# Optimization experiments

Hardware: AMD Instinct MI355X
Metric: run time of the kernel (lower is better)

Reference implementation:

```python
import jax, jax.numpy as jnp
import numpy as np


def setup_inputs() -> dict:
    key = jax.random.key(0)
    x = jax.random.normal(key, (8192, 1024), dtype=jnp.float32)
    return {"x": x}


def reference(x):
    # attn_scores = x @ x.T  -> [N, N]
    scores = jnp.einsum('nd,md->nm', x, x)
    # softmax over last dim (stable)
    weights = jax.nn.softmax(scores, axis=-1)
    # context = weights @ x -> [N, d]
    return jnp.einsum('nm,md->nd', weights, x)
```

## Files before the change

### kernel.cpp

```cpp
#include <hip/hip_runtime.h>
#include <hip/hip_bf16.h>
#include <cstdint>

#define NROWS 8192
#define DDIM  1024
#define QBLK  32
#define KVT   128
#define DC    64
#define NW    8
#define NITER (NROWS / KVT)
#define NDC   (DDIM / DC)
#define LOG2E 1.44269504088896340736f

typedef __attribute__((ext_vector_type(4))) float f32x4;
typedef __attribute__((ext_vector_type(8))) short bf16x8;
typedef unsigned short u16;

__device__ __forceinline__ u16 f2bf(float f) {
  uint32_t u = __builtin_bit_cast(uint32_t, f);
  uint32_t r = u + 0x7FFFu + ((u >> 16) & 1u);
  return (u16)(r >> 16);
}

__global__ __launch_bounds__(256) void prep_kernel(const float* __restrict__ x,
                                                   u16* __restrict__ xbf,
                                                   u16* __restrict__ xbfT) {
  __shared__ __align__(16) u16 T[64][72];
  const int t = threadIdx.x;
  const int n0 = blockIdx.x * 64;
  const int d0 = blockIdx.y * 64;
#pragma unroll
  for (int rr = 0; rr < 4; ++rr) {
    const int row = (t >> 4) + rr * 16;
    const int c4 = (t & 15) * 4;
    const float4 v = *reinterpret_cast<const float4*>(&x[(size_t)(n0 + row) * DDIM + d0 + c4]);
    ushort4 b;
    b.x = f2bf(v.x); b.y = f2bf(v.y); b.z = f2bf(v.z); b.w = f2bf(v.w);
    *reinterpret_cast<ushort4*>(&xbf[(size_t)(n0 + row) * DDIM + d0 + c4]) = b;
    *reinterpret_cast<ushort4*>(&T[row][c4]) = b;
  }
  __syncthreads();
#pragma unroll
  for (int rr = 0; rr < 4; ++rr) {
    const int drow = (t >> 4) + rr * 16;
    const int nc = (t & 15) * 4;
    ushort4 o;
    o.x = T[nc + 0][drow]; o.y = T[nc + 1][drow];
    o.z = T[nc + 2][drow]; o.w = T[nc + 3][drow];
    *reinterpret_cast<ushort4*>(&xbfT[(size_t)(d0 + drow) * NROWS + n0 + nc]) = o;
  }
}

__global__ __launch_bounds__(512, 2) void attn_kernel(const u16* __restrict__ xbf,
                                                      const u16* __restrict__ xbfT,
                                                      float* __restrict__ out) {
  __shared__ __align__(16) u16 Qs[2][QBLK][DC + 8];
  __shared__ __align__(16) u16 Ks[2][KVT][DC + 8];
  __shared__ __align__(16) u16 Ps[QBLK][KVT + 8];
  __shared__ float smax[NW][QBLK];
  __shared__ float ssum[NW][QBLK];

  const int tid = threadIdx.x;
  const int w = tid >> 6;
  const int lane = tid & 63;
  const int g = lane >> 4;
  const int ln16 = lane & 15;
  const int j = lane & 31;
  const int q0 = blockIdx.x * QBLK;

  const int kr = tid >> 2, kc = (tid & 3) * 16;
  const int qr = tid >> 4, qc = (tid & 15) * 4;

  int4 rk0, rk1; ushort4 rq;

  auto load_chunk = [&](int t_, int dc_) {
    const size_t ko = (size_t)(t_ * KVT + kr) * DDIM + dc_ * DC + kc;
    rk0 = *reinterpret_cast<const int4*>(&xbf[ko]);
    rk1 = *reinterpret_cast<const int4*>(&xbf[ko + 8]);
    const size_t qo = (size_t)(q0 + qr) * DDIM + dc_ * DC + qc;
    rq = *reinterpret_cast<const ushort4*>(&xbf[qo]);
  };
  auto write_chunk = [&](int buf) {
    *reinterpret_cast<int4*>(&Ks[buf][kr][kc]) = rk0;
    *reinterpret_cast<int4*>(&Ks[buf][kr][kc + 8]) = rk1;
    *reinterpret_cast<ushort4*>(&Qs[buf][qr][qc]) = rq;
  };

  f32x4 oacc[2][8];
#pragma unroll
  for (int f = 0; f < 2; ++f)
#pragma unroll
    for (int c = 0; c < 8; ++c) oacc[f][c] = (f32x4){0.f, 0.f, 0.f, 0.f};
  float m_run = -INFINITY, l_run = 0.0f;

  load_chunk(0, 0);

  for (int t = 0; t < NITER; ++t) {
    f32x4 sacc[2] = {{0.f,0.f,0.f,0.f},{0.f,0.f,0.f,0.f}};
    for (int dc = 0; dc < NDC; ++dc) {
      const int buf = dc & 1;
      write_chunk(buf);
      if (dc + 1 < NDC) load_chunk(t, dc + 1);
      else if (t + 1 < NITER) load_chunk(t + 1, 0);
      __syncthreads();
#pragma unroll
      for (int kk = 0; kk < 2; ++kk) {
        const int kq = kk * 32 + g * 8;
        bf16x8 a0 = *reinterpret_cast<const bf16x8*>(&Qs[buf][ln16][kq]);
        bf16x8 a1 = *reinterpret_cast<const bf16x8*>(&Qs[buf][16 + ln16][kq]);
        bf16x8 b  = *reinterpret_cast<const bf16x8*>(&Ks[buf][w * 16 + ln16][kq]);
        sacc[0] = __builtin_amdgcn_mfma_f32_16x16x32_bf16(a0, b, sacc[0], 0, 0, 0);
        sacc[1] = __builtin_amdgcn_mfma_f32_16x16x32_bf16(a1, b, sacc[1], 0, 0, 0);
      }
    }

    float rmx[2][4];
#pragma unroll
    for (int f = 0; f < 2; ++f)
#pragma unroll
      for (int r = 0; r < 4; ++r) {
        float v = sacc[f][r];
        v = fmaxf(v, __shfl_xor(v, 1, 16));
        v = fmaxf(v, __shfl_xor(v, 2, 16));
        v = fmaxf(v, __shfl_xor(v, 4, 16));
        v = fmaxf(v, __shfl_xor(v, 8, 16));
        rmx[f][r] = v;
      }
    if (ln16 == 0) {
#pragma unroll
      for (int f = 0; f < 2; ++f)
#pragma unroll
        for (int r = 0; r < 4; ++r) smax[w][f * 16 + g * 4 + r] = rmx[f][r];
    }
    __syncthreads();
    float tm = smax[0][j];
#pragma unroll
    for (int wv = 1; wv < NW; ++wv) tm = fmaxf(tm, smax[wv][j]);
    const float mnew = fmaxf(m_run, tm);
    const float alpha = exp2f((m_run - mnew) * LOG2E);
    m_run = mnew;

    float mrow[2][4], arow[2][4];
#pragma unroll
    for (int f = 0; f < 2; ++f)
#pragma unroll
      for (int r = 0; r < 4; ++r) {
        const int row = f * 16 + g * 4 + r;
        mrow[f][r] = __shfl(mnew, row);
        arow[f][r] = __shfl(alpha, row);
      }

    float prb[2][4], rs[2][4];
#pragma unroll
    for (int f = 0; f < 2; ++f)
#pragma unroll
      for (int r = 0; r < 4; ++r) {
        const float p = exp2f((sacc[f][r] - mrow[f][r]) * LOG2E);
        prb[f][r] = p;
        float s = p;
        s += __shfl_xor(s, 1, 16);
        s += __shfl_xor(s, 2, 16);
        s += __shfl_xor(s, 4, 16);
        s += __shfl_xor(s, 8, 16);
        rs[f][r] = s;
      }
    if (ln16 == 0) {
#pragma unroll
      for (int f = 0; f < 2; ++f)
#pragma unroll
        for (int r = 0; r < 4; ++r) ssum[w][f * 16 + g * 4 + r] = rs[f][r];
    }
#pragma unroll
    for (int f = 0; f < 2; ++f)
#pragma unroll
      for (int r = 0; r < 4; ++r)
        Ps[f * 16 + g * 4 + r][w * 16 + ln16] = f2bf(prb[f][r]);
    __syncthreads();

    float ts = ssum[0][j];
#pragma unroll
    for (int wv = 1; wv < NW; ++wv) ts += ssum[wv][j];
    l_run = l_run * alpha + ts;

#pragma unroll
    for (int f = 0; f < 2; ++f)
#pragma unroll
      for (int cf = 0; cf < 8; ++cf)
#pragma unroll
        for (int r = 0; r < 4; ++r) oacc[f][cf][r] *= arow[f][r];

    const int kvb = t * KVT;
#pragma unroll
    for (int kk = 0; kk < 4; ++kk) {
      bf16x8 pa0 = *reinterpret_cast<const bf16x8*>(&Ps[ln16][kk * 32 + g * 8]);
      bf16x8 pa1 = *reinterpret_cast<const bf16x8*>(&Ps[16 + ln16][kk * 32 + g * 8]);
#pragma unroll
      for (int cf = 0; cf < 8; ++cf) {
        const int c = w * 128 + cf * 16 + ln16;
        const int4 vv = *reinterpret_cast<const int4*>(
            &xbfT[(size_t)c * NROWS + kvb + kk * 32 + g * 8]);
        const bf16x8 vb = __builtin_bit_cast(bf16x8, vv);
        oacc[0][cf] = __builtin_amdgcn_mfma_f32_16x16x32_bf16(pa0, vb, oacc[0][cf], 0, 0, 0);
        oacc[1][cf] = __builtin_amdgcn_mfma_f32_16x16x32_bf16(pa1, vb, oacc[1][cf], 0, 0, 0);
      }
    }
  }

  const float rinv = 1.0f / l_run;
  float rrow[2][4];
#pragma unroll
  for (int f = 0; f < 2; ++f)
#pragma unroll
    for (int r = 0; r < 4; ++r) rrow[f][r] = __shfl(rinv, f * 16 + g * 4 + r);
#pragma unroll
  for (int f = 0; f < 2; ++f)
#pragma unroll
    for (int cf = 0; cf < 8; ++cf)
#pragma unroll
      for (int r = 0; r < 4; ++r) {
        const int row = q0 + f * 16 + g * 4 + r;
        const int c = w * 128 + cf * 16 + ln16;
        out[(size_t)row * DDIM + c] = oacc[f][cf][r] * rrow[f][r];
      }
}

extern "C" void kernel_launch(void* const* d_in, const int* in_sizes, int n_in,
                              void* d_out, int out_size, void* d_ws, size_t ws_size,
                              hipStream_t stream) {
  const float* x = (const float*)d_in[0];
  u16* xbf  = (u16*)d_ws;
  u16* xbfT = xbf + (size_t)NROWS * DDIM;
  float* out = (float*)d_out;

  hipLaunchKernelGGL(prep_kernel, dim3(NROWS / 64, DDIM / 64), dim3(256), 0, stream,
                     x, xbf, xbfT);
  hipLaunchKernelGGL(attn_kernel, dim3(NROWS / QBLK), dim3(512), 0, stream,
                     xbf, xbfT, out);
}
```

Baseline: 997.0 us.

## Halve query block, keep full Q tile resident in LDS, batch V loads

Reduces the query block from 32 to 16 rows, which doubles the grid to 512 blocks and raises the occupancy target to 4 blocks per CU. The whole 16x1024 Q tile is now loaded into LDS once, so the per-chunk Q streaming is gone. In the PV loop, all eight V fragments are loaded before the MFMAs run, and the MFMA section is wrapped in raised wave priority. The trade-off is that each K/V tile now serves half as many query rows, so global and L2 traffic for K and V roughly doubles.

```diff
diff --git a/kernel.cpp b/kernel.cpp
--- a/kernel.cpp
+++ b/kernel.cpp
@@ -4,7 +4,7 @@
 
 #define NROWS 8192
 #define DDIM  1024
-#define QBLK  32
+#define QBLK  16
 #define KVT   128
 #define DC    64
 #define NW    8
@@ -51,10 +51,10 @@
   }
 }
 
-__global__ __launch_bounds__(512, 2) void attn_kernel(const u16* __restrict__ xbf,
+__global__ __launch_bounds__(512, 4) void attn_kernel(const u16* __restrict__ xbf,
                                                       const u16* __restrict__ xbfT,
                                                       float* __restrict__ out) {
-  __shared__ __align__(16) u16 Qs[2][QBLK][DC + 8];
+  __shared__ __align__(16) u16 Qf[QBLK][DDIM + 8];
   __shared__ __align__(16) u16 Ks[2][KVT][DC + 8];
   __shared__ __align__(16) u16 Ps[QBLK][KVT + 8];
   __shared__ float smax[NW][QBLK];
@@ -65,38 +65,39 @@
   const int lane = tid & 63;
   const int g = lane >> 4;
   const int ln16 = lane & 15;
-  const int j = lane & 31;
   const int q0 = blockIdx.x * QBLK;
 
+  {
+    const int qr = tid >> 5;
+    const int qc0 = (tid & 31) * 32;
+#pragma unroll
+    for (int i = 0; i < 4; ++i) {
+      const int4 v = *reinterpret_cast<const int4*>(&xbf[(size_t)(q0 + qr) * DDIM + qc0 + i * 8]);
+      *reinterpret_cast<int4*>(&Qf[qr][qc0 + i * 8]) = v;
+    }
+  }
+
   const int kr = tid >> 2, kc = (tid & 3) * 16;
-  const int qr = tid >> 4, qc = (tid & 15) * 4;
-
-  int4 rk0, rk1; ushort4 rq;
-
+  int4 rk0, rk1;
   auto load_chunk = [&](int t_, int dc_) {
     const size_t ko = (size_t)(t_ * KVT + kr) * DDIM + dc_ * DC + kc;
     rk0 = *reinterpret_cast<const int4*>(&xbf[ko]);
     rk1 = *reinterpret_cast<const int4*>(&xbf[ko + 8]);
-    const size_t qo = (size_t)(q0 + qr) * DDIM + dc_ * DC + qc;
-    rq = *reinterpret_cast<const ushort4*>(&xbf[qo]);
   };
   auto write_chunk = [&](int buf) {
     *reinterpret_cast<int4*>(&Ks[buf][kr][kc]) = rk0;
     *reinterpret_cast<int4*>(&Ks[buf][kr][kc + 8]) = rk1;
-    *reinterpret_cast<ushort4*>(&Qs[buf][qr][qc]) = rq;
   };
 
-  f32x4 oacc[2][8];
-#pragma unroll
-  for (int f = 0; f < 2; ++f)
-#pragma unroll
-    for (int c = 0; c < 8; ++c) oacc[f][c] = (f32x4){0.f, 0.f, 0.f, 0.f};
+  f32x4 oacc[8];
+#pragma unroll
+  for (int c = 0; c < 8; ++c) oacc[c] = (f32x4){0.f, 0.f, 0.f, 0.f};
   float m_run = -INFINITY, l_run = 0.0f;
 
   load_chunk(0, 0);
 
   for (int t = 0; t < NITER; ++t) {
-    f32x4 sacc[2] = {{0.f,0.f,0.f,0.f},{0.f,0.f,0.f,0.f}};
+    f32x4 sacc = {0.f, 0.f, 0.f, 0.f};
     for (int dc = 0; dc < NDC; ++dc) {
       const int buf = dc & 1;
       write_chunk(buf);
@@ -105,123 +106,105 @@
       __syncthreads();
 #pragma unroll
       for (int kk = 0; kk < 2; ++kk) {
-        const int kq = kk * 32 + g * 8;
-        bf16x8 a0 = *reinterpret_cast<const bf16x8*>(&Qs[buf][ln16][kq]);
-        bf16x8 a1 = *reinterpret_cast<const bf16x8*>(&Qs[buf][16 + ln16][kq]);
-        bf16x8 b  = *reinterpret_cast<const bf16x8*>(&Ks[buf][w * 16 + ln16][kq]);
-        sacc[0] = __builtin_amdgcn_mfma_f32_16x16x32_bf16(a0, b, sacc[0], 0, 0, 0);
-        sacc[1] = __builtin_amdgcn_mfma_f32_16x16x32_bf16(a1, b, sacc[1], 0, 0, 0);
+        bf16x8 a = *reinterpret_cast<const bf16x8*>(&Qf[ln16][dc * DC + kk * 32 + g * 8]);
+        bf16x8 b = *reinterpret_cast<const bf16x8*>(&Ks[buf][w * 16 + ln16][kk * 32 + g * 8]);
+        sacc = __builtin_amdgcn_mfma_f32_16x16x32_bf16(a, b, sacc, 0, 0, 0);
       }
     }
 
-    float rmx[2][4];
-#pragma unroll
-    for (int f = 0; f < 2; ++f)
-#pragma unroll
-      for (int r = 0; r < 4; ++r) {
-        float v = sacc[f][r];
-        v = fmaxf(v, __shfl_xor(v, 1, 16));
-        v = fmaxf(v, __shfl_xor(v, 2, 16));
-        v = fmaxf(v, __shfl_xor(v, 4, 16));
-        v = fmaxf(v, __shfl_xor(v, 8, 16));
-        rmx[f][r] = v;
-      }
+    float rmx[4];
+#pragma unroll
+    for (int r = 0; r < 4; ++r) {
+      float v = sacc[r];
+      v = fmaxf(v, __shfl_xor(v, 1, 16));
+      v = fmaxf(v, __shfl_xor(v, 2, 16));
+      v = fmaxf(v, __shfl_xor(v, 4, 16));
+      v = fmaxf(v, __shfl_xor(v, 8, 16));
+      rmx[r] = v;
+    }
     if (ln16 == 0) {
 #pragma unroll
-      for (int f = 0; f < 2; ++f)
-#pragma unroll
-        for (int r = 0; r < 4; ++r) smax[w][f * 16 + g * 4 + r] = rmx[f][r];
+      for (int r = 0; r < 4; ++r) smax[w][g * 4 + r] = rmx[r];
     }
     __syncthreads();
-    float tm = smax[0][j];
-#pragma unroll
-    for (int wv = 1; wv < NW; ++wv) tm = fmaxf(tm, smax[wv][j]);
+    float tm = smax[0][ln16];
+#pragma unroll
+    for (int wv = 1; wv < NW; ++wv) tm = fmaxf(tm, smax[wv][ln16]);
     const float mnew = fmaxf(m_run, tm);
     const float alpha = exp2f((m_run - mnew) * LOG2E);
     m_run = mnew;
 
-    float mrow[2][4], arow[2][4];
-#pragma unroll
-    for (int f = 0; f < 2; ++f)
-#pragma unroll
-      for (int r = 0; r < 4; ++r) {
-        const int row = f * 16 + g * 4 + r;
-        mrow[f][r] = __shfl(mnew, row);
-        arow[f][r] = __shfl(alpha, row);
-      }
-
-    float prb[2][4], rs[2][4];
-#pragma unroll
-    for (int f = 0; f < 2; ++f)
-#pragma unroll
-      for (int r = 0; r < 4; ++r) {
-        const float p = exp2f((sacc[f][r] - mrow[f][r]) * LOG2E);
-        prb[f][r] = p;
-        float s = p;
-        s += __shfl_xor(s, 1, 16);
-        s += __shfl_xor(s, 2, 16);
-        s += __shfl_xor(s, 4, 16);
-        s += __shfl_xor(s, 8, 16);
-        rs[f][r] = s;
-      }
+    float mrow[4], arow[4];
+#pragma unroll
+    for (int r = 0; r < 4; ++r) {
+      mrow[r] = __shfl(mnew, g * 4 + r);
+      arow[r] = __shfl(alpha, g * 4 + r);
+    }
+
+    float prb[4], rs[4];
+#pragma unroll
+    for (int r = 0; r < 4; ++r) {
+      const float p = exp2f((sacc[r] - mrow[r]) * LOG2E);
+      prb[r] = p;
+      float s = p;
+      s += __shfl_xor(s, 1, 16);
+      s += __shfl_xor(s, 2, 16);
+      s += __shfl_xor(s, 4, 16);
+      s += __shfl_xor(s, 8, 16);
+      rs[r] = s;
+    }
     if (ln16 == 0) {
 #pragma unroll
-      for (int f = 0; f < 2; ++f)
-#pragma unroll
-        for (int r = 0; r < 4; ++r) ssum[w][f * 16 + g * 4 + r] = rs[f][r];
-    }
-#pragma unroll
-    for (int f = 0; f < 2; ++f)
-#pragma unroll
-      for (int r = 0; r < 4; ++r)
-        Ps[f * 16 + g * 4 + r][w * 16 + ln16] = f2bf(prb[f][r]);
+      for (int r = 0; r < 4; ++r) ssum[w][g * 4 + r] = rs[r];
+    }
+#pragma unroll
+    for (int r = 0; r < 4; ++r)
+      Ps[g * 4 + r][w * 16 + ln16] = f2bf(prb[r]);
     __syncthreads();
 
-    float ts = ssum[0][j];
-#pragma unroll
-    for (int wv = 1; wv < NW; ++wv) ts += ssum[wv][j];
+    float ts = ssum[0][ln16];
+#pragma unroll
+    for (int wv = 1; wv < NW; ++wv) ts += ssum[wv][ln16];
     l_run = l_run * alpha + ts;
 
 #pragma unroll
-    for (int f = 0; f < 2; ++f)
-#pragma unroll
-      for (int cf = 0; cf < 8; ++cf)
-#pragma unroll
-        for (int r = 0; r < 4; ++r) oacc[f][cf][r] *= arow[f][r];
+    for (int cf = 0; cf < 8; ++cf)
+#pragma unroll
+      for (int r = 0; r < 4; ++r) oacc[cf][r] *= arow[r];
 
     const int kvb = t * KVT;
 #pragma unroll
     for (int kk = 0; kk < 4; ++kk) {
-      bf16x8 pa0 = *reinterpret_cast<const bf16x8*>(&Ps[ln16][kk * 32 + g * 8]);
-      bf16x8 pa1 = *reinterpret_cast<const bf16x8*>(&Ps[16 + ln16][kk * 32 + g * 8]);
+      int4 vv[8];
 #pragma unroll
       for (int cf = 0; cf < 8; ++cf) {
         const int c = w * 128 + cf * 16 + ln16;
-        const int4 vv = *reinterpret_cast<const int4*>(
+        vv[cf] = *reinterpret_cast<const int4*>(
             &xbfT[(size_t)c * NROWS + kvb + kk * 32 + g * 8]);
-        const bf16x8 vb = __builtin_bit_cast(bf16x8, vv);
-        oacc[0][cf] = __builtin_amdgcn_mfma_f32_16x16x32_bf16(pa0, vb, oacc[0][cf], 0, 0, 0);
-        oacc[1][cf] = __builtin_amdgcn_mfma_f32_16x16x32_bf16(pa1, vb, oacc[1][cf], 0, 0, 0);
       }
+      const bf16x8 pa = *reinterpret_cast<const bf16x8*>(&Ps[ln16][kk * 32 + g * 8]);
+      __builtin_amdgcn_s_setprio(1);
+#pragma unroll
+      for (int cf = 0; cf < 8; ++cf) {
+        oacc[cf] = __builtin_amdgcn_mfma_f32_16x16x32_bf16(
+            pa, __builtin_bit_cast(bf16x8, vv[cf]), oacc[cf], 0, 0, 0);
+      }
+      __builtin_amdgcn_s_setprio(0);
     }
   }
 
   const float rinv = 1.0f / l_run;
-  float rrow[2][4];
-#pragma unroll
-  for (int f = 0; f < 2; ++f)
-#pragma unroll
-    for (int r = 0; r < 4; ++r) rrow[f][r] = __shfl(rinv, f * 16 + g * 4 + r);
-#pragma unroll
-  for (int f = 0; f < 2; ++f)
-#pragma unroll
-    for (int cf = 0; cf < 8; ++cf)
-#pragma unroll
-      for (int r = 0; r < 4; ++r) {
-        const int row = q0 + f * 16 + g * 4 + r;
-        const int c = w * 128 + cf * 16 + ln16;
-        out[(size_t)row * DDIM + c] = oacc[f][cf][r] * rrow[f][r];
-      }
+  float rrow[4];
+#pragma unroll
+  for (int r = 0; r < 4; ++r) rrow[r] = __shfl(rinv, g * 4 + r);
+#pragma unroll
+  for (int cf = 0; cf < 8; ++cf)
+#pragma unroll
+    for (int r = 0; r < 4; ++r) {
+      const int row = q0 + g * 4 + r;
+      const int c = w * 128 + cf * 16 + ln16;
+      out[(size_t)row * DDIM + c] = oacc[cf][r] * rrow[r];
+    }
 }
 
 extern "C" void kernel_launch(void* const* d_in, const int* in_sizes, int n_in,
```

Measured after the change: 1.676 ms. 68.1% more time.

## Keep Q block resident in LDS and stream K/V from global into registers

Applied to the files above, without the earlier changes.

The full 32x1024 query block is loaded once into shared memory. The per-chunk double-buffered K staging through LDS, with its barrier on every 64-wide chunk, is replaced by direct global loads of K fragments into a 4-deep register prefetch ring. The KV tile doubles to 256, so each wave computes two score fragments, and V loads for the PV product are double-buffered in registers with raised MFMA priority. This removes most of the shared-memory traffic and the per-chunk barriers in the QK^T phase. In exchange it adds register pressure and relies on the L2 cache for K reuse across waves and blocks, and the larger LDS footprint may reduce occupancy.

```diff
diff --git a/kernel.cpp b/kernel.cpp
--- a/kernel.cpp
+++ b/kernel.cpp
@@ -5,11 +5,11 @@
 #define NROWS 8192
 #define DDIM  1024
 #define QBLK  32
-#define KVT   128
-#define DC    64
+#define KVT   256
 #define NW    8
 #define NITER (NROWS / KVT)
-#define NDC   (DDIM / DC)
+#define KS_S  (DDIM / 32)
+#define KS_PV (KVT / 32)
 #define LOG2E 1.44269504088896340736f
 
 typedef __attribute__((ext_vector_type(4))) float f32x4;
@@ -21,6 +21,7 @@
   uint32_t r = u + 0x7FFFu + ((u >> 16) & 1u);
   return (u16)(r >> 16);
 }
+__device__ __forceinline__ bf16x8 asbf(int4 v) { return __builtin_bit_cast(bf16x8, v); }
 
 __global__ __launch_bounds__(256) void prep_kernel(const float* __restrict__ x,
                                                    u16* __restrict__ xbf,
@@ -54,8 +55,7 @@
 __global__ __launch_bounds__(512, 2) void attn_kernel(const u16* __restrict__ xbf,
                                                       const u16* __restrict__ xbfT,
                                                       float* __restrict__ out) {
-  __shared__ __align__(16) u16 Qs[2][QBLK][DC + 8];
-  __shared__ __align__(16) u16 Ks[2][KVT][DC + 8];
+  __shared__ __align__(16) u16 Qf[QBLK][DDIM + 8];
   __shared__ __align__(16) u16 Ps[QBLK][KVT + 8];
   __shared__ float smax[NW][QBLK];
   __shared__ float ssum[NW][QBLK];
@@ -68,69 +68,69 @@
   const int j = lane & 31;
   const int q0 = blockIdx.x * QBLK;
 
-  const int kr = tid >> 2, kc = (tid & 3) * 16;
-  const int qr = tid >> 4, qc = (tid & 15) * 4;
-
-  int4 rk0, rk1; ushort4 rq;
-
-  auto load_chunk = [&](int t_, int dc_) {
-    const size_t ko = (size_t)(t_ * KVT + kr) * DDIM + dc_ * DC + kc;
-    rk0 = *reinterpret_cast<const int4*>(&xbf[ko]);
-    rk1 = *reinterpret_cast<const int4*>(&xbf[ko + 8]);
-    const size_t qo = (size_t)(q0 + qr) * DDIM + dc_ * DC + qc;
-    rq = *reinterpret_cast<const ushort4*>(&xbf[qo]);
-  };
-  auto write_chunk = [&](int buf) {
-    *reinterpret_cast<int4*>(&Ks[buf][kr][kc]) = rk0;
-    *reinterpret_cast<int4*>(&Ks[buf][kr][kc + 8]) = rk1;
-    *reinterpret_cast<ushort4*>(&Qs[buf][qr][qc]) = rq;
-  };
+  {
+    const int qr = tid >> 4;
+    const int qc0 = (tid & 15) * 64;
+#pragma unroll
+    for (int i = 0; i < 8; ++i) {
+      const int4 v = *reinterpret_cast<const int4*>(&xbf[(size_t)(q0 + qr) * DDIM + qc0 + i * 8]);
+      *reinterpret_cast<int4*>(&Qf[qr][qc0 + i * 8]) = v;
+    }
+  }
+  __syncthreads();
 
   f32x4 oacc[2][8];
 #pragma unroll
-  for (int f = 0; f < 2; ++f)
-#pragma unroll
-    for (int c = 0; c < 8; ++c) oacc[f][c] = (f32x4){0.f, 0.f, 0.f, 0.f};
+  for (int qf = 0; qf < 2; ++qf)
+#pragma unroll
+    for (int c = 0; c < 8; ++c) oacc[qf][c] = (f32x4){0.f, 0.f, 0.f, 0.f};
   float m_run = -INFINITY, l_run = 0.0f;
 
-  load_chunk(0, 0);
-
   for (int t = 0; t < NITER; ++t) {
-    f32x4 sacc[2] = {{0.f,0.f,0.f,0.f},{0.f,0.f,0.f,0.f}};
-    for (int dc = 0; dc < NDC; ++dc) {
-      const int buf = dc & 1;
-      write_chunk(buf);
-      if (dc + 1 < NDC) load_chunk(t, dc + 1);
-      else if (t + 1 < NITER) load_chunk(t + 1, 0);
-      __syncthreads();
-#pragma unroll
-      for (int kk = 0; kk < 2; ++kk) {
-        const int kq = kk * 32 + g * 8;
-        bf16x8 a0 = *reinterpret_cast<const bf16x8*>(&Qs[buf][ln16][kq]);
-        bf16x8 a1 = *reinterpret_cast<const bf16x8*>(&Qs[buf][16 + ln16][kq]);
-        bf16x8 b  = *reinterpret_cast<const bf16x8*>(&Ks[buf][w * 16 + ln16][kq]);
-        sacc[0] = __builtin_amdgcn_mfma_f32_16x16x32_bf16(a0, b, sacc[0], 0, 0, 0);
-        sacc[1] = __builtin_amdgcn_mfma_f32_16x16x32_bf16(a1, b, sacc[1], 0, 0, 0);
-      }
+    const int kvb = t * KVT;
+
+    const u16* kbase = xbf + (size_t)(kvb + w * 32) * DDIM + g * 8;
+    f32x4 sacc[2][2] = {{{0.f,0.f,0.f,0.f},{0.f,0.f,0.f,0.f}},
+                        {{0.f,0.f,0.f,0.f},{0.f,0.f,0.f,0.f}}};
+    int4 kb[4][2];
+#pragma unroll
+    for (int p = 0; p < 3; ++p) {
+      kb[p][0] = *reinterpret_cast<const int4*>(kbase + (size_t)ln16 * DDIM + p * 32);
+      kb[p][1] = *reinterpret_cast<const int4*>(kbase + (size_t)(16 + ln16) * DDIM + p * 32);
+    }
+#pragma unroll
+    for (int ks = 0; ks < KS_S; ++ks) {
+      if (ks + 3 < KS_S) {
+        kb[(ks + 3) & 3][0] = *reinterpret_cast<const int4*>(kbase + (size_t)ln16 * DDIM + (ks + 3) * 32);
+        kb[(ks + 3) & 3][1] = *reinterpret_cast<const int4*>(kbase + (size_t)(16 + ln16) * DDIM + (ks + 3) * 32);
+      }
+      const bf16x8 a0 = *reinterpret_cast<const bf16x8*>(&Qf[ln16][ks * 32 + g * 8]);
+      const bf16x8 a1 = *reinterpret_cast<const bf16x8*>(&Qf[16 + ln16][ks * 32 + g * 8]);
+      const bf16x8 b0 = asbf(kb[ks & 3][0]);
+      const bf16x8 b1 = asbf(kb[ks & 3][1]);
+      sacc[0][0] = __builtin_amdgcn_mfma_f32_16x16x32_bf16(a0, b0, sacc[0][0], 0, 0, 0);
+      sacc[1][0] = __builtin_amdgcn_mfma_f32_16x16x32_bf16(a1, b0, sacc[1][0], 0, 0, 0);
+      sacc[0][1] = __builtin_amdgcn_mfma_f32_16x16x32_bf16(a0, b1, sacc[0][1], 0, 0, 0);
+      sacc[1][1] = __builtin_amdgcn_mfma_f32_16x16x32_bf16(a1, b1, sacc[1][1], 0, 0, 0);
     }
 
     float rmx[2][4];
 #pragma unroll
-    for (int f = 0; f < 2; ++f)
-#pragma unroll
-      for (int r = 0; r < 4; ++r) {
-        float v = sacc[f][r];
+    for (int qf = 0; qf < 2; ++qf)
+#pragma unroll
+      for (int r = 0; r < 4; ++r) {
+        float v = fmaxf(sacc[qf][0][r], sacc[qf][1][r]);
         v = fmaxf(v, __shfl_xor(v, 1, 16));
         v = fmaxf(v, __shfl_xor(v, 2, 16));
         v = fmaxf(v, __shfl_xor(v, 4, 16));
         v = fmaxf(v, __shfl_xor(v, 8, 16));
-        rmx[f][r] = v;
+        rmx[qf][r] = v;
       }
     if (ln16 == 0) {
 #pragma unroll
-      for (int f = 0; f < 2; ++f)
-#pragma unroll
-        for (int r = 0; r < 4; ++r) smax[w][f * 16 + g * 4 + r] = rmx[f][r];
+      for (int qf = 0; qf < 2; ++qf)
+#pragma unroll
+        for (int r = 0; r < 4; ++r) smax[w][qf * 16 + g * 4 + r] = rmx[qf][r];
     }
     __syncthreads();
     float tm = smax[0][j];
@@ -142,85 +142,89 @@
 
     float mrow[2][4], arow[2][4];
 #pragma unroll
-    for (int f = 0; f < 2; ++f)
-#pragma unroll
-      for (int r = 0; r < 4; ++r) {
-        const int row = f * 16 + g * 4 + r;
-        mrow[f][r] = __shfl(mnew, row);
-        arow[f][r] = __shfl(alpha, row);
-      }
-
-    float prb[2][4], rs[2][4];
-#pragma unroll
-    for (int f = 0; f < 2; ++f)
-#pragma unroll
-      for (int r = 0; r < 4; ++r) {
-        const float p = exp2f((sacc[f][r] - mrow[f][r]) * LOG2E);
-        prb[f][r] = p;
-        float s = p;
+    for (int qf = 0; qf < 2; ++qf)
+#pragma unroll
+      for (int r = 0; r < 4; ++r) {
+        mrow[qf][r] = __shfl(mnew, qf * 16 + g * 4 + r);
+        arow[qf][r] = __shfl(alpha, qf * 16 + g * 4 + r);
+      }
+
+    float rs[2][4];
+#pragma unroll
+    for (int qf = 0; qf < 2; ++qf)
+#pragma unroll
+      for (int r = 0; r < 4; ++r) {
+        const float p0 = exp2f((sacc[qf][0][r] - mrow[qf][r]) * LOG2E);
+        const float p1 = exp2f((sacc[qf][1][r] - mrow[qf][r]) * LOG2E);
+        Ps[qf * 16 + g * 4 + r][w * 32 + ln16]      = f2bf(p0);
+        Ps[qf * 16 + g * 4 + r][w * 32 + 16 + ln16] = f2bf(p1);
+        float s = p0 + p1;
         s += __shfl_xor(s, 1, 16);
         s += __shfl_xor(s, 2, 16);
         s += __shfl_xor(s, 4, 16);
         s += __shfl_xor(s, 8, 16);
-        rs[f][r] = s;
+        rs[qf][r] = s;
       }
     if (ln16 == 0) {
 #pragma unroll
-      for (int f = 0; f < 2; ++f)
-#pragma unroll
-        for (int r = 0; r < 4; ++r) ssum[w][f * 16 + g * 4 + r] = rs[f][r];
-    }
-#pragma unroll
-    for (int f = 0; f < 2; ++f)
-#pragma unroll
-      for (int r = 0; r < 4; ++r)
-        Ps[f * 16 + g * 4 + r][w * 16 + ln16] = f2bf(prb[f][r]);
+      for (int qf = 0; qf < 2; ++qf)
+#pragma unroll
+        for (int r = 0; r < 4; ++r) ssum[w][qf * 16 + g * 4 + r] = rs[qf][r];
+    }
     __syncthreads();
-
     float ts = ssum[0][j];
 #pragma unroll
     for (int wv = 1; wv < NW; ++wv) ts += ssum[wv][j];
     l_run = l_run * alpha + ts;
 
 #pragma unroll
-    for (int f = 0; f < 2; ++f)
+    for (int qf = 0; qf < 2; ++qf)
 #pragma unroll
       for (int cf = 0; cf < 8; ++cf)
 #pragma unroll
-        for (int r = 0; r < 4; ++r) oacc[f][cf][r] *= arow[f][r];
-
-    const int kvb = t * KVT;
-#pragma unroll
-    for (int kk = 0; kk < 4; ++kk) {
-      bf16x8 pa0 = *reinterpret_cast<const bf16x8*>(&Ps[ln16][kk * 32 + g * 8]);
-      bf16x8 pa1 = *reinterpret_cast<const bf16x8*>(&Ps[16 + ln16][kk * 32 + g * 8]);
+        for (int r = 0; r < 4; ++r) oacc[qf][cf][r] *= arow[qf][r];
+
+    const u16* vbase = xbfT + (size_t)(w * 128 + ln16) * NROWS + kvb + g * 8;
+    int4 vv[2][8];
+#pragma unroll
+    for (int cf = 0; cf < 8; ++cf)
+      vv[0][cf] = *reinterpret_cast<const int4*>(vbase + (size_t)(cf * 16) * NROWS);
+#pragma unroll
+    for (int ks = 0; ks < KS_PV; ++ks) {
+      const int cur = ks & 1;
+      if (ks + 1 < KS_PV) {
+#pragma unroll
+        for (int cf = 0; cf < 8; ++cf)
+          vv[cur ^ 1][cf] = *reinterpret_cast<const int4*>(
+              vbase + (size_t)(cf * 16) * NROWS + (ks + 1) * 32);
+      }
+      const bf16x8 pa0 = *reinterpret_cast<const bf16x8*>(&Ps[ln16][ks * 32 + g * 8]);
+      const bf16x8 pa1 = *reinterpret_cast<const bf16x8*>(&Ps[16 + ln16][ks * 32 + g * 8]);
+      __builtin_amdgcn_s_setprio(1);
 #pragma unroll
       for (int cf = 0; cf < 8; ++cf) {
-        const int c = w * 128 + cf * 16 + ln16;
-        const int4 vv = *reinterpret_cast<const int4*>(
-            &xbfT[(size_t)c * NROWS + kvb + kk * 32 + g * 8]);
-        const bf16x8 vb = __builtin_bit_cast(bf16x8, vv);
-        oacc[0][cf] = __builtin_amdgcn_mfma_f32_16x16x32_bf16(pa0, vb, oacc[0][cf], 0, 0, 0);
-        oacc[1][cf] = __builtin_amdgcn_mfma_f32_16x16x32_bf16(pa1, vb, oacc[1][cf], 0, 0, 0);
-      }
+        oacc[0][cf] = __builtin_amdgcn_mfma_f32_16x16x32_bf16(pa0, asbf(vv[cur][cf]), oacc[0][cf], 0, 0, 0);
+        oacc[1][cf] = __builtin_amdgcn_mfma_f32_16x16x32_bf16(pa1, asbf(vv[cur][cf]), oacc[1][cf], 0, 0, 0);
+      }
+      __builtin_amdgcn_s_setprio(0);
     }
   }
 
   const float rinv = 1.0f / l_run;
   float rrow[2][4];
 #pragma unroll
-  for (int f = 0; f < 2; ++f)
-#pragma unroll
-    for (int r = 0; r < 4; ++r) rrow[f][r] = __shfl(rinv, f * 16 + g * 4 + r);
-#pragma unroll
-  for (int f = 0; f < 2; ++f)
+  for (int qf = 0; qf < 2; ++qf)
+#pragma unroll
+    for (int r = 0; r < 4; ++r) rrow[qf][r] = __shfl(rinv, qf * 4 == 0 ? g * 4 + r : qf * 16 + g * 4 + r);
+#pragma unroll
+  for (int qf = 0; qf < 2; ++qf)
 #pragma unroll
     for (int cf = 0; cf < 8; ++cf)
 #pragma unroll
       for (int r = 0; r < 4; ++r) {
-        const int row = q0 + f * 16 + g * 4 + r;
+        const int row = q0 + qf * 16 + g * 4 + r;
         const int c = w * 128 + cf * 16 + ln16;
-        out[(size_t)row * DDIM + c] = oacc[f][cf][r] * rrow[f][r];
+        out[(size_t)row * DDIM + c] = oacc[qf][cf][r] * rrow[qf][r];
       }
 }
 
```

Result: slower. 1.060 ms (+6.3%).
